# Optimization experiments

Measured on AMD Instinct MI355X. Metric: run time of the kernel, lower is better.

The kernel has to match this reference:

```python
import jax, jax.numpy as jnp
import numpy as np

N_NODES = 50000
N_EDGES = 600000
D = 128
L = 3


def setup_inputs() -> dict:
    key = jax.random.key(0)
    ks = jax.random.split(key, 6)
    x = jax.random.normal(ks[0], (N_NODES, D), dtype=jnp.float32)
    edge_index = jax.random.randint(ks[1], (2, N_EDGES), 0, N_NODES, dtype=jnp.int64)
    # Glorot-ish scale for 128x128 linears
    s = 1.0 / np.sqrt(D)
    W_l = jax.random.normal(ks[2], (L, D, D), dtype=jnp.float32) * s
    b_l = jnp.zeros((L, D), dtype=jnp.float32)
    W_r = jax.random.normal(ks[3], (L, D, D), dtype=jnp.float32) * s
    W_out = jax.random.normal(ks[4], (D, 1), dtype=jnp.float32) * s
    b_out = jnp.zeros((1,), dtype=jnp.float32)
    return {"x": x, "edge_index": edge_index, "W_l": W_l, "b_l": b_l,
            "W_r": W_r, "W_out": W_out, "b_out": b_out}


def reference(x, edge_index, W_l, b_l, W_r, W_out, b_out):
    # PyG SAGEConv (aggr='mean', root_weight=True):
    #   out_i = lin_l(mean_{j: (j->i)} x_j) + lin_r(x_i)
    src = edge_index[0]
    dst = edge_index[1]
    n = x.shape[0]
    deg = jax.ops.segment_sum(jnp.ones(src.shape, x.dtype), dst, num_segments=n)
    inv_deg = (1.0 / jnp.maximum(deg, 1.0))[:, None]  # [N,1]
    h = x
    for i in range(W_l.shape[0]):  # fixed small layer count
        agg = jax.ops.segment_sum(h[src], dst, num_segments=n) * inv_deg  # [N,D]
        h = agg @ W_l[i] + b_l[i] + h @ W_r[i]
        h = jax.nn.relu(h)  # dropout is identity at eval (p=0.0)
    return (h @ W_out + b_out)[:, 0]  # squeeze(-1) -> [N]
```

## Files before the change

### kernel.cpp

```cpp
#include <hip/hip_runtime.h>

#define N_NODES 50000
#define N_EDGES 600000
#define D 128
#define NLAYERS 3
#define CSR_CAP (N_EDGES + 3 * N_NODES)

typedef __attribute__((ext_vector_type(8))) short short8;
typedef __attribute__((ext_vector_type(4))) float floatx4;

__device__ __forceinline__ float bf_lo(unsigned u) { return __uint_as_float(u << 16); }
__device__ __forceinline__ float bf_hi(unsigned u) { return __uint_as_float(u & 0xffff0000u); }
__device__ __forceinline__ unsigned short f2bf(float f) {
    unsigned u = __float_as_uint(f);
    return (unsigned short)((u + 0x7fffu + ((u >> 16) & 1u)) >> 16);
}


#define CVT_A (N_NODES * D / 4)
#define CVT_B (NLAYERS * D * 256)
#define CVT_TOTAL (CVT_A + CVT_B + N_NODES)

__global__ void cvt_init_kernel(const float* __restrict__ x, const float* __restrict__ Wl,
                                const float* __restrict__ Wr,
                                unsigned short* __restrict__ xb,
                                unsigned short* __restrict__ hb1,
                                unsigned short* __restrict__ hb2,
                                unsigned short* __restrict__ WtF,
                                int* __restrict__ deg, int* __restrict__ cursor,
                                int* __restrict__ counter) {
    int i = blockIdx.x * blockDim.x + threadIdx.x;
    if (i < CVT_A) {
        float4 v = ((const float4*)x)[i];
        ushort4 o;
        o.x = f2bf(v.x); o.y = f2bf(v.y); o.z = f2bf(v.z); o.w = f2bf(v.w);
        ((ushort4*)xb)[i] = o;
    } else if (i < CVT_A + CVT_B) {
        int t = i - CVT_A;
        int l = t >> 15;
        int r = t & 32767;
        int f = r >> 3;
        int ii = r & 7;
        int jkt = f >> 6;
        int lane = f & 63;
        int j = jkt >> 3;
        int kt = jkt & 7;
        int half = lane & 15;
        int quad = lane >> 4;
        int n = j * 16 + half;
        int k = kt * 32 + quad * 8 + ii;
        float v = (k < D) ? Wl[(size_t)l * D * D + (size_t)k * D + n]
                          : Wr[(size_t)l * D * D + (size_t)(k - D) * D + n];
        WtF[t] = f2bf(v);
    } else if (i < CVT_TOTAL) {
        int j = i - (CVT_A + CVT_B);
        deg[j] = 0;
        cursor[j] = 0;
        if (j == 0) counter[0] = 0;
        if (j < D) {
            xb[(size_t)N_NODES * D + j] = 0;
            hb1[(size_t)N_NODES * D + j] = 0;
            hb2[(size_t)N_NODES * D + j] = 0;
        }
    }
}


__global__ void hist_kernel(const int* __restrict__ dst, int* __restrict__ deg) {
    int e = blockIdx.x * blockDim.x + threadIdx.x;
    if (e < N_EDGES) atomicAdd(&deg[dst[e]], 1);
}

__global__ void alloc_kernel(const int* __restrict__ deg, int* __restrict__ counter,
                             int* __restrict__ row_start, float* __restrict__ inv_deg,
                             int* __restrict__ csr_src) {
    int i = blockIdx.x * blockDim.x + threadIdx.x;
    int lane = threadIdx.x & 63;
    int d = (i < N_NODES) ? deg[i] : 0;
    int pd = (d + 3) & ~3;
    int v = pd;
    #pragma unroll
    for (int off = 1; off < 64; off <<= 1) {
        int t = __shfl_up(v, off, 64);
        if (lane >= off) v += t;
    }
    int total = __shfl(v, 63, 64);
    int base = 0;
    if (lane == 63) base = atomicAdd(counter, total);
    base = __shfl(base, 63, 64);
    if (i < N_NODES) {
        int rs = base + v - pd;
        row_start[i] = rs;
        inv_deg[i] = 1.0f / fmaxf((float)d, 1.0f);
        for (int k = d; k < pd; k++) csr_src[rs + k] = N_NODES;
    }
}

__global__ void fill_kernel(const int* __restrict__ src, const int* __restrict__ dst,
                            const int* __restrict__ row_start, int* __restrict__ cursor,
                            int* __restrict__ csr_src) {
    int e = blockIdx.x * blockDim.x + threadIdx.x;
    if (e < N_EDGES) {
        int d_ = dst[e];
        int pos = atomicAdd(&cursor[d_], 1);
        csr_src[row_start[d_] + pos] = src[e];
    }
}


template <bool LAST>
__global__ __launch_bounds__(256) void fused_layer_kernel(
    const unsigned short* __restrict__ hin,
    const int* __restrict__ row_start, const int* __restrict__ deg,
    const int* __restrict__ csr_src, const float* __restrict__ inv_deg,
    const unsigned short* __restrict__ WtF, const float* __restrict__ bias,
    unsigned short* __restrict__ hout,
    const float* __restrict__ Wout, const float* __restrict__ bout,
    float* __restrict__ out) {
    __shared__ unsigned short a_s[32 * 256];
    __shared__ unsigned short c_s[32][136];

    int m0 = blockIdx.x * 32;
    int tid = threadIdx.x;

    #pragma unroll
    for (int it = 0; it < 2; ++it) {
        int t = it * 256 + tid;
        int rl = t >> 4;
        int c = t & 15;
        int row = min(m0 + rl, N_NODES - 1);
        uint4 v = *((const uint4*)(hin + (size_t)row * D + c * 8));
        int chunk = (16 + c) ^ (rl & 7);
        *((uint4*)&a_s[rl * 256 + chunk * 8]) = v;
    }

    {
        int grp = tid >> 4;
        int q = tid & 15;
        for (int half_ = 0; half_ < 2; ++half_) {
            int nl = grp + half_ * 16;
            int node = m0 + nl;
            float a[8] = {0.f, 0.f, 0.f, 0.f, 0.f, 0.f, 0.f, 0.f};
            float b[8] = {0.f, 0.f, 0.f, 0.f, 0.f, 0.f, 0.f, 0.f};
            float w = 0.f;
            if (node < N_NODES) {
                int d = deg[node];
                int pd = (d + 3) & ~3;
                int beg = row_start[node];
                for (int e = beg; e < beg + pd; e += 16) {
                    int cnt = min(beg + pd - e, 16);
                    int idx = csr_src[e + min(q, cnt - 1)];
                    for (int j = 0; j < cnt; j += 4) {
                        int s0 = __shfl(idx, j + 0, 16);
                        int s1 = __shfl(idx, j + 1, 16);
                        int s2 = __shfl(idx, j + 2, 16);
                        int s3 = __shfl(idx, j + 3, 16);
                        uint4 v0 = *((const uint4*)(hin + (size_t)s0 * D + q * 8));
                        uint4 v1 = *((const uint4*)(hin + (size_t)s1 * D + q * 8));
                        uint4 v2 = *((const uint4*)(hin + (size_t)s2 * D + q * 8));
                        uint4 v3 = *((const uint4*)(hin + (size_t)s3 * D + q * 8));
                        a[0] += bf_lo(v0.x); a[1] += bf_hi(v0.x);
                        a[2] += bf_lo(v0.y); a[3] += bf_hi(v0.y);
                        a[4] += bf_lo(v0.z); a[5] += bf_hi(v0.z);
                        a[6] += bf_lo(v0.w); a[7] += bf_hi(v0.w);
                        b[0] += bf_lo(v1.x); b[1] += bf_hi(v1.x);
                        b[2] += bf_lo(v1.y); b[3] += bf_hi(v1.y);
                        b[4] += bf_lo(v1.z); b[5] += bf_hi(v1.z);
                        b[6] += bf_lo(v1.w); b[7] += bf_hi(v1.w);
                        a[0] += bf_lo(v2.x); a[1] += bf_hi(v2.x);
                        a[2] += bf_lo(v2.y); a[3] += bf_hi(v2.y);
                        a[4] += bf_lo(v2.z); a[5] += bf_hi(v2.z);
                        a[6] += bf_lo(v2.w); a[7] += bf_hi(v2.w);
                        b[0] += bf_lo(v3.x); b[1] += bf_hi(v3.x);
                        b[2] += bf_lo(v3.y); b[3] += bf_hi(v3.y);
                        b[4] += bf_lo(v3.z); b[5] += bf_hi(v3.z);
                        b[6] += bf_lo(v3.w); b[7] += bf_hi(v3.w);
                    }
                }
                w = inv_deg[node];
            }
            uint4 o;
            o.x = (unsigned)f2bf((a[0] + b[0]) * w) | ((unsigned)f2bf((a[1] + b[1]) * w) << 16);
            o.y = (unsigned)f2bf((a[2] + b[2]) * w) | ((unsigned)f2bf((a[3] + b[3]) * w) << 16);
            o.z = (unsigned)f2bf((a[4] + b[4]) * w) | ((unsigned)f2bf((a[5] + b[5]) * w) << 16);
            o.w = (unsigned)f2bf((a[6] + b[6]) * w) | ((unsigned)f2bf((a[7] + b[7]) * w) << 16);
            int chunk = q ^ (nl & 7);
            *((uint4*)&a_s[nl * 256 + chunk * 8]) = o;
        }
    }
    __syncthreads();

    int wv = tid >> 6;
    int lane = tid & 63;
    int half = lane & 15;
    int quad = lane >> 4;

    floatx4 acc[2][2];
    #pragma unroll
    for (int mt = 0; mt < 2; mt++)
        #pragma unroll
        for (int jj = 0; jj < 2; jj++)
            acc[mt][jj] = (floatx4){0.f, 0.f, 0.f, 0.f};

    const short8* Bf = (const short8*)WtF;
    #pragma unroll
    for (int kt = 0; kt < 8; kt++) {
        int ch = (kt * 4 + quad) ^ (half & 7);
        short8 a0 = *((const short8*)&a_s[half * 256 + ch * 8]);
        short8 a1 = *((const short8*)&a_s[(16 + half) * 256 + ch * 8]);
        #pragma unroll
        for (int jj = 0; jj < 2; jj++) {
            int j = wv * 2 + jj;
            short8 b = Bf[(j * 8 + kt) * 64 + lane];
            acc[0][jj] = __builtin_amdgcn_mfma_f32_16x16x32_bf16(a0, b, acc[0][jj], 0, 0, 0);
            acc[1][jj] = __builtin_amdgcn_mfma_f32_16x16x32_bf16(a1, b, acc[1][jj], 0, 0, 0);
        }
    }

    if (!LAST) {
        #pragma unroll
        for (int jj = 0; jj < 2; jj++) {
            int col = (wv * 2 + jj) * 16 + half;
            float bv = bias[col];
            #pragma unroll
            for (int mt = 0; mt < 2; mt++)
                #pragma unroll
                for (int r = 0; r < 4; r++)
                    c_s[mt * 16 + quad * 4 + r][col] = f2bf(fmaxf(acc[mt][jj][r] + bv, 0.f));
        }
        __syncthreads();
        #pragma unroll
        for (int it = 0; it < 2; ++it) {
            int t = it * 256 + tid;
            int rl = t >> 4;
            int c = t & 15;
            int row = m0 + rl;
            if (row < N_NODES)
                *((uint4*)(hout + (size_t)row * D + c * 8)) = *((const uint4*)&c_s[rl][c * 8]);
        }
    } else {
        float* red = (float*)&c_s[0][0];
        float vout[2][4] = {{0.f, 0.f, 0.f, 0.f}, {0.f, 0.f, 0.f, 0.f}};
        #pragma unroll
        for (int jj = 0; jj < 2; jj++) {
            int col = (wv * 2 + jj) * 16 + half;
            float bv = bias[col];
            float wo = Wout[col];
            #pragma unroll
            for (int mt = 0; mt < 2; mt++)
                #pragma unroll
                for (int r = 0; r < 4; r++)
                    vout[mt][r] += fmaxf(acc[mt][jj][r] + bv, 0.f) * wo;
        }
        #pragma unroll
        for (int off = 1; off < 16; off <<= 1) {
            #pragma unroll
            for (int mt = 0; mt < 2; mt++)
                #pragma unroll
                for (int r = 0; r < 4; r++)
                    vout[mt][r] += __shfl_xor(vout[mt][r], off, 64);
        }
        if (half == 0) {
            #pragma unroll
            for (int mt = 0; mt < 2; mt++)
                #pragma unroll
                for (int r = 0; r < 4; r++)
                    red[(mt * 16 + quad * 4 + r) * 4 + wv] = vout[mt][r];
        }
        __syncthreads();
        if (tid < 32) {
            int row = m0 + tid;
            if (row < N_NODES)
                out[row] = red[tid * 4 + 0] + red[tid * 4 + 1] +
                           red[tid * 4 + 2] + red[tid * 4 + 3] + bout[0];
        }
    }
}


extern "C" void kernel_launch(void* const* d_in, const int* in_sizes, int n_in,
                              void* d_out, int out_size, void* d_ws, size_t ws_size,
                              hipStream_t stream) {
    const float* x     = (const float*)d_in[0];
    const int*   edge  = (const int*)d_in[1];
    const float* W_l   = (const float*)d_in[2];
    const float* b_l   = (const float*)d_in[3];
    const float* W_r   = (const float*)d_in[4];
    const float* W_out = (const float*)d_in[5];
    const float* b_out = (const float*)d_in[6];
    float* out = (float*)d_out;

    char* ws = (char*)d_ws;
    size_t off = 0;
    auto alloc = [&](size_t bytes) -> void* {
        void* p = ws + off;
        off += (bytes + 255) & ~(size_t)255;
        return p;
    };
    unsigned short* xb  = (unsigned short*)alloc((size_t)(N_NODES + 1) * D * 2);
    unsigned short* hb1 = (unsigned short*)alloc((size_t)(N_NODES + 1) * D * 2);
    unsigned short* hb2 = (unsigned short*)alloc((size_t)(N_NODES + 1) * D * 2);
    unsigned short* WtF = (unsigned short*)alloc((size_t)NLAYERS * D * 256 * 2);
    int*   deg       = (int*)alloc((size_t)N_NODES * sizeof(int));
    int*   row_start = (int*)alloc((size_t)N_NODES * sizeof(int));
    int*   cursor    = (int*)alloc((size_t)N_NODES * sizeof(int));
    float* inv_deg   = (float*)alloc((size_t)N_NODES * sizeof(float));
    int*   csr_src   = (int*)alloc((size_t)CSR_CAP * sizeof(int));
    int*   counter   = (int*)alloc(256);

    const int* src = edge;
    const int* dst = edge + N_EDGES;

    cvt_init_kernel<<<(CVT_TOTAL + 255) / 256, 256, 0, stream>>>(
        x, W_l, W_r, xb, hb1, hb2, WtF, deg, cursor, counter);
    hist_kernel<<<(N_EDGES + 255) / 256, 256, 0, stream>>>(dst, deg);
    alloc_kernel<<<(N_NODES + 255) / 256, 256, 0, stream>>>(deg, counter, row_start, inv_deg, csr_src);
    fill_kernel<<<(N_EDGES + 255) / 256, 256, 0, stream>>>(src, dst, row_start, cursor, csr_src);

    const int grid = (N_NODES + 31) / 32;

    fused_layer_kernel<false><<<grid, 256, 0, stream>>>(
        xb, row_start, deg, csr_src, inv_deg, WtF, b_l, hb1, W_out, b_out, out);
    fused_layer_kernel<false><<<grid, 256, 0, stream>>>(
        hb1, row_start, deg, csr_src, inv_deg, WtF + (size_t)1 * D * 256, b_l + 1 * D,
        hb2, W_out, b_out, out);
    fused_layer_kernel<true><<<grid, 256, 0, stream>>>(
        hb2, row_start, deg, csr_src, inv_deg, WtF + (size_t)2 * D * 256, b_l + 2 * D,
        hb1, W_out, b_out, out);
}
```

Measured before the change: 242.6 us.

## Restructure neighbor gather: one wave per node, quads split edges, prefetch indices

The aggregation phase is reorganized so each wave processes 8 nodes in sequence. Within a wave the four 16-lane quads gather different edges of the same node in parallel and are combined with cross-quad shuffles. Per-node metadata is loaded once per wave and the next node's CSR indices are prefetched. The self-feature tile load is issued before the gather and stored to shared memory afterwards, to overlap its latency. This is meant to raise memory-level parallelism for low-degree nodes and hide index-load latency, at the cost of extra shuffle reductions and a serialized per-node loop.

```diff
diff --git a/kernel.cpp b/kernel.cpp
--- a/kernel.cpp
+++ b/kernel.cpp
@@ -14,6 +14,13 @@
 __device__ __forceinline__ unsigned short f2bf(float f) {
     unsigned u = __float_as_uint(f);
     return (unsigned short)((u + 0x7fffu + ((u >> 16) & 1u)) >> 16);
+}
+
+__device__ __forceinline__ void acc8(float* a, uint4 v) {
+    a[0] += bf_lo(v.x); a[1] += bf_hi(v.x);
+    a[2] += bf_lo(v.y); a[3] += bf_hi(v.y);
+    a[4] += bf_lo(v.z); a[5] += bf_hi(v.z);
+    a[6] += bf_lo(v.w); a[7] += bf_hi(v.w);
 }
 
 
@@ -122,78 +129,115 @@
 
     int m0 = blockIdx.x * 32;
     int tid = threadIdx.x;
-
-    #pragma unroll
-    for (int it = 0; it < 2; ++it) {
-        int t = it * 256 + tid;
-        int rl = t >> 4;
-        int c = t & 15;
-        int row = min(m0 + rl, N_NODES - 1);
-        uint4 v = *((const uint4*)(hin + (size_t)row * D + c * 8));
-        int chunk = (16 + c) ^ (rl & 7);
-        *((uint4*)&a_s[rl * 256 + chunk * 8]) = v;
-    }
-
-    {
-        int grp = tid >> 4;
-        int q = tid & 15;
-        for (int half_ = 0; half_ < 2; ++half_) {
-            int nl = grp + half_ * 16;
-            int node = m0 + nl;
-            float a[8] = {0.f, 0.f, 0.f, 0.f, 0.f, 0.f, 0.f, 0.f};
-            float b[8] = {0.f, 0.f, 0.f, 0.f, 0.f, 0.f, 0.f, 0.f};
-            float w = 0.f;
-            if (node < N_NODES) {
-                int d = deg[node];
-                int pd = (d + 3) & ~3;
-                int beg = row_start[node];
-                for (int e = beg; e < beg + pd; e += 16) {
-                    int cnt = min(beg + pd - e, 16);
-                    int idx = csr_src[e + min(q, cnt - 1)];
-                    for (int j = 0; j < cnt; j += 4) {
-                        int s0 = __shfl(idx, j + 0, 16);
-                        int s1 = __shfl(idx, j + 1, 16);
-                        int s2 = __shfl(idx, j + 2, 16);
-                        int s3 = __shfl(idx, j + 3, 16);
-                        uint4 v0 = *((const uint4*)(hin + (size_t)s0 * D + q * 8));
-                        uint4 v1 = *((const uint4*)(hin + (size_t)s1 * D + q * 8));
-                        uint4 v2 = *((const uint4*)(hin + (size_t)s2 * D + q * 8));
-                        uint4 v3 = *((const uint4*)(hin + (size_t)s3 * D + q * 8));
-                        a[0] += bf_lo(v0.x); a[1] += bf_hi(v0.x);
-                        a[2] += bf_lo(v0.y); a[3] += bf_hi(v0.y);
-                        a[4] += bf_lo(v0.z); a[5] += bf_hi(v0.z);
-                        a[6] += bf_lo(v0.w); a[7] += bf_hi(v0.w);
-                        b[0] += bf_lo(v1.x); b[1] += bf_hi(v1.x);
-                        b[2] += bf_lo(v1.y); b[3] += bf_hi(v1.y);
-                        b[4] += bf_lo(v1.z); b[5] += bf_hi(v1.z);
-                        b[6] += bf_lo(v1.w); b[7] += bf_hi(v1.w);
-                        a[0] += bf_lo(v2.x); a[1] += bf_hi(v2.x);
-                        a[2] += bf_lo(v2.y); a[3] += bf_hi(v2.y);
-                        a[4] += bf_lo(v2.z); a[5] += bf_hi(v2.z);
-                        a[6] += bf_lo(v2.w); a[7] += bf_hi(v2.w);
-                        b[0] += bf_lo(v3.x); b[1] += bf_hi(v3.x);
-                        b[2] += bf_lo(v3.y); b[3] += bf_hi(v3.y);
-                        b[4] += bf_lo(v3.z); b[5] += bf_hi(v3.z);
-                        b[6] += bf_lo(v3.w); b[7] += bf_hi(v3.w);
-                    }
-                }
-                w = inv_deg[node];
-            }
-            uint4 o;
-            o.x = (unsigned)f2bf((a[0] + b[0]) * w) | ((unsigned)f2bf((a[1] + b[1]) * w) << 16);
-            o.y = (unsigned)f2bf((a[2] + b[2]) * w) | ((unsigned)f2bf((a[3] + b[3]) * w) << 16);
-            o.z = (unsigned)f2bf((a[4] + b[4]) * w) | ((unsigned)f2bf((a[5] + b[5]) * w) << 16);
-            o.w = (unsigned)f2bf((a[6] + b[6]) * w) | ((unsigned)f2bf((a[7] + b[7]) * w) << 16);
-            int chunk = q ^ (nl & 7);
-            *((uint4*)&a_s[nl * 256 + chunk * 8]) = o;
-        }
-    }
-    __syncthreads();
-
     int wv = tid >> 6;
     int lane = tid & 63;
-    int half = lane & 15;
+    int lane15 = lane & 15;
     int quad = lane >> 4;
+
+    uint4 st0, st1;
+    int strow0, stcol0, strow1, stcol1;
+    {
+        int t0 = tid;
+        strow0 = t0 >> 4; stcol0 = t0 & 15;
+        int row0 = min(m0 + strow0, N_NODES - 1);
+        st0 = *((const uint4*)(hin + (size_t)row0 * D + stcol0 * 8));
+        int t1 = 256 + tid;
+        strow1 = t1 >> 4; stcol1 = t1 & 15;
+        int row1 = min(m0 + strow1, N_NODES - 1);
+        st1 = *((const uint4*)(hin + (size_t)row1 * D + stcol1 * 8));
+    }
+
+    {
+        int nodeBase = m0 + wv * 8;
+        int sel = lane & 7;
+        int metaIdx = min(nodeBase + sel, N_NODES - 1);
+        int rs_l = row_start[metaIdx];
+        int dg_l = (nodeBase + sel < N_NODES) ? deg[metaIdx] : 0;
+        float w_l = inv_deg[metaIdx];
+
+        int beg_n = __shfl(rs_l, 0, 8);
+        int pd_n  = (__shfl(dg_l, 0, 8) + 3) & ~3;
+        int idx_next = csr_src[min(beg_n + min(lane15, max(min(pd_n, 16) - 1, 0)),
+                                   CSR_CAP - 1)];
+
+        #pragma unroll 1
+        for (int n = 0; n < 8; n++) {
+            int beg = beg_n;
+            int pd  = pd_n;
+            int idx = idx_next;
+            int n2 = min(n + 1, 7);
+            beg_n = __shfl(rs_l, n2, 8);
+            pd_n  = (__shfl(dg_l, n2, 8) + 3) & ~3;
+            idx_next = csr_src[min(beg_n + min(lane15, max(min(pd_n, 16) - 1, 0)),
+                                   CSR_CAP - 1)];
+
+            float a[8] = {0.f, 0.f, 0.f, 0.f, 0.f, 0.f, 0.f, 0.f};
+
+            {
+                int cnt = min(pd, 16);
+                int nb = cnt >> 2;
+                int s0 = __shfl(idx, quad, 16);
+                int s1 = __shfl(idx, 4 + quad, 16);
+                int s2 = __shfl(idx, 8 + quad, 16);
+                int s3 = __shfl(idx, 12 + quad, 16);
+                uint4 v0, v1, v2, v3;
+                if (nb > 0) v0 = *((const uint4*)(hin + (size_t)s0 * D + lane15 * 8));
+                if (nb > 1) v1 = *((const uint4*)(hin + (size_t)s1 * D + lane15 * 8));
+                if (nb > 2) v2 = *((const uint4*)(hin + (size_t)s2 * D + lane15 * 8));
+                if (nb > 3) v3 = *((const uint4*)(hin + (size_t)s3 * D + lane15 * 8));
+                if (nb > 0) acc8(a, v0);
+                if (nb > 1) acc8(a, v1);
+                if (nb > 2) acc8(a, v2);
+                if (nb > 3) acc8(a, v3);
+            }
+            for (int e = beg + 16; e < beg + pd; e += 16) {
+                int cnt = min(beg + pd - e, 16);
+                int idx2 = csr_src[e + min(lane15, cnt - 1)];
+                int nb = cnt >> 2;
+                int s0 = __shfl(idx2, quad, 16);
+                int s1 = __shfl(idx2, 4 + quad, 16);
+                int s2 = __shfl(idx2, 8 + quad, 16);
+                int s3 = __shfl(idx2, 12 + quad, 16);
+                uint4 v0, v1, v2, v3;
+                if (nb > 0) v0 = *((const uint4*)(hin + (size_t)s0 * D + lane15 * 8));
+                if (nb > 1) v1 = *((const uint4*)(hin + (size_t)s1 * D + lane15 * 8));
+                if (nb > 2) v2 = *((const uint4*)(hin + (size_t)s2 * D + lane15 * 8));
+                if (nb > 3) v3 = *((const uint4*)(hin + (size_t)s3 * D + lane15 * 8));
+                if (nb > 0) acc8(a, v0);
+                if (nb > 1) acc8(a, v1);
+                if (nb > 2) acc8(a, v2);
+                if (nb > 3) acc8(a, v3);
+            }
+
+            #pragma unroll
+            for (int i = 0; i < 8; i++) {
+                a[i] += __shfl_xor(a[i], 16, 64);
+                a[i] += __shfl_xor(a[i], 32, 64);
+            }
+
+            float w = __shfl(w_l, n, 8);
+            if (quad == 0) {
+                int nl = wv * 8 + n;
+                uint4 o;
+                o.x = (unsigned)f2bf(a[0] * w) | ((unsigned)f2bf(a[1] * w) << 16);
+                o.y = (unsigned)f2bf(a[2] * w) | ((unsigned)f2bf(a[3] * w) << 16);
+                o.z = (unsigned)f2bf(a[4] * w) | ((unsigned)f2bf(a[5] * w) << 16);
+                o.w = (unsigned)f2bf(a[6] * w) | ((unsigned)f2bf(a[7] * w) << 16);
+                int chunk = lane15 ^ (nl & 7);
+                *((uint4*)&a_s[nl * 256 + chunk * 8]) = o;
+            }
+        }
+    }
+
+    {
+        int chunk0 = (16 + stcol0) ^ (strow0 & 7);
+        *((uint4*)&a_s[strow0 * 256 + chunk0 * 8]) = st0;
+        int chunk1 = (16 + stcol1) ^ (strow1 & 7);
+        *((uint4*)&a_s[strow1 * 256 + chunk1 * 8]) = st1;
+    }
+    __syncthreads();
+
+    int half = lane15;
 
     floatx4 acc[2][2];
     #pragma unroll
```

After: 243.9 us. No clear change (+0.5%).
